# Kernel tuning notes

Measured on AMD Instinct MI355X. Metric: run time of the kernel, lower is better.

Reference implementation:

```python
import jax, jax.numpy as jnp
import numpy as np

B, C, H, W = 8, 256, 64, 64
HEADS, PTS = 8, 4
HD = C // HEADS
CIN_G, CIN_S, COUT = 1024, 320, 320


def _sine_pe(c, h, w):
    # LoFTR-style 2D sinusoidal position encoding, returns [C,H,W]
    pe = np.zeros((c, h, w), dtype=np.float32)
    y = np.broadcast_to(np.arange(h, dtype=np.float32)[None, :, None], (1, h, w))
    x = np.broadcast_to(np.arange(w, dtype=np.float32)[None, None, :], (1, h, w))
    div = np.exp(np.arange(0, c // 2, 2, dtype=np.float32) * (-np.log(10000.0) / (c // 2)))[:, None, None]
    pe[0::4] = np.sin(x * div)
    pe[1::4] = np.cos(x * div)
    pe[2::4] = np.sin(y * div)
    pe[3::4] = np.cos(y * div)
    return jnp.asarray(pe)


def _ref_points(h, w):
    # faithful to source: meshgrid over (W,H) 'ij', stack (col,row), flatten w-major
    rows = np.linspace(0, 1, w, dtype=np.float32)
    cols = np.linspace(0, 1, h, dtype=np.float32)
    R, Cg = np.meshgrid(rows, cols, indexing='ij')  # [W,H]
    return jnp.asarray(np.stack([Cg, R], -1).reshape(-1, 2))  # [W*H,2]


PE = _sine_pe(C, H, W)
RP = _ref_points(H, W)


def conv1x1(x, w, b):
    return jnp.einsum('bchw,oc->bohw', x, w) + b[None, :, None, None]


def deform_attn(qf, vf, vp_w, vp_b, so_w, so_b, aw_w, aw_b, op_w, op_b):
    # qf: [B,Nq,C]  vf: [B,Nv,C]  (single level, H x W value map)
    Bn, Nq, Cc = qf.shape
    v = (vf @ vp_w + vp_b).reshape(Bn, -1, HEADS, HD).transpose(0, 2, 1, 3)  # [B,h,Nv,hd]
    off = (qf @ so_w + so_b).reshape(Bn, Nq, HEADS, PTS, 2)
    aw = jax.nn.softmax((qf @ aw_w + aw_b).reshape(Bn, Nq, HEADS, PTS), axis=-1)
    loc = RP[None, :, None, None, :] + off / jnp.array([W, H], qf.dtype)  # [B,Nq,h,P,2]
    # grid_sample align_corners=False, zero padding
    px = loc[..., 0] * W - 0.5
    py = loc[..., 1] * H - 0.5
    x0 = jnp.floor(px).astype(jnp.int32)
    y0 = jnp.floor(py).astype(jnp.int32)
    wx = px - x0
    wy = py - y0
    out = jnp.zeros((Bn, HEADS, Nq, PTS, HD), qf.dtype)
    for dx, dy, wgt in ((0, 0, (1 - wx) * (1 - wy)), (1, 0, wx * (1 - wy)),
                        (0, 1, (1 - wx) * wy), (1, 1, wx * wy)):
        xi = x0 + dx
        yi = y0 + dy
        valid = ((xi >= 0) & (xi < W) & (yi >= 0) & (yi < H)).astype(qf.dtype)
        idx = jnp.clip(yi, 0, H - 1) * W + jnp.clip(xi, 0, W - 1)  # [B,Nq,h,P]
        idx_h = idx.transpose(0, 2, 1, 3).reshape(Bn, HEADS, Nq * PTS)
        g = jnp.take_along_axis(v, idx_h[..., None], axis=2).reshape(Bn, HEADS, Nq, PTS, HD)
        out = out + g * (wgt * valid).transpose(0, 2, 1, 3)[..., None]
    o = (out * aw.transpose(0, 2, 1, 3)[..., None]).sum(3)  # [B,h,Nq,hd]
    o = o.transpose(0, 2, 1, 3).reshape(Bn, Nq, Cc)
    return o @ op_w + op_b + qf  # mmcv: output_proj + identity (dropout=eval)


def cross_attn(q, value, vp_w, vp_b, so_w, so_b, aw_w, aw_b, op_w, op_b):
    qp = q + PE[None]  # query += pe
    qf = qp.reshape(qp.shape[0], C, H * W).transpose(0, 2, 1)
    vf = value.reshape(value.shape[0], C, H * W).transpose(0, 2, 1)
    o = deform_attn(qf, vf, vp_w, vp_b, so_w, so_b, aw_w, aw_b, op_w, op_b)
    o = o.transpose(0, 2, 1).reshape(qp.shape)
    return o + qp


def setup_inputs() -> dict:
    key = jax.random.key(0)
    ks = jax.random.split(key, 40)
    inp = {}
    inp['ground'] = jax.random.normal(ks[0], (B, CIN_G, H, W), jnp.float32)
    inp['sat'] = jax.random.normal(ks[1], (B, CIN_S, H, W), jnp.float32)
    inp['osm'] = jax.random.normal(ks[2], (B, CIN_S, H, W), jnp.float32)
    i = [3]
    def p(name, shape, scale=0.02):
        inp[name] = jax.random.normal(ks[i[0]], shape, jnp.float32) * scale
        i[0] += 1
    p('gc_w', (C, CIN_G)); p('gc_b', (C,))
    p('sc_w', (C, CIN_S)); p('sc_b', (C,))
    p('up_w', (COUT, C)); p('up_b', (COUT,))
    p('a_w1', (C, 64)); p('a_b1', (64,))
    p('a_w2', (64, 1)); p('a_b2', (1,))
    for pre in ('sat_', 'osm_'):
        p(pre + 'vp_w', (C, C)); p(pre + 'vp_b', (C,))
        p(pre + 'so_w', (C, HEADS * PTS * 2)); p(pre + 'so_b', (HEADS * PTS * 2,))
        p(pre + 'aw_w', (C, HEADS * PTS)); p(pre + 'aw_b', (HEADS * PTS,))
        p(pre + 'op_w', (C, C)); p(pre + 'op_b', (C,))
    inp['index'] = 0
    return inp


def reference(ground, sat, osm, gc_w, gc_b, sc_w, sc_b, up_w, up_b,
              a_w1, a_b1, a_w2, a_b2,
              sat_vp_w, sat_vp_b, sat_so_w, sat_so_b, sat_aw_w, sat_aw_b, sat_op_w, sat_op_b,
              osm_vp_w, osm_vp_b, osm_so_w, osm_so_b, osm_aw_w, osm_aw_b, osm_op_w, osm_op_b,
              index):
    del index  # params for index=0 already selected
    g = conv1x1(ground, gc_w, gc_b)
    s = conv1x1(sat, sc_w, sc_b)
    o = conv1x1(osm, sc_w, sc_b)  # source bug: osm projected with sat_convs
    gf = g.reshape(B, C, H * W).transpose(0, 2, 1)
    alpha = jax.nn.sigmoid(jax.nn.relu(gf @ a_w1 + a_b1) @ a_w2 + a_b2)  # [B,Nq,1]
    a = alpha.mean(axis=1)[:, :, None, None]  # [B,1,1,1]
    sat_out = cross_attn(g, s, sat_vp_w, sat_vp_b, sat_so_w, sat_so_b, sat_aw_w, sat_aw_b, sat_op_w, sat_op_b)
    # torch in-place `query += pe` inside ca_sat mutates `ground`, so ca_osm sees g + PE
    osm_out = cross_attn(g + PE[None], o, osm_vp_w, osm_vp_b, osm_so_w, osm_so_b, osm_aw_w, osm_aw_b, osm_op_w, osm_op_b)
    fused = a * sat_out + (1.0 - a) * osm_out
    return conv1x1(fused, up_w, up_b), a
```

## Files before the change

kernel.cpp:

```cpp
#include <hip/hip_runtime.h>
#include <cstddef>
#include <cstdint>

#define NB 8
#define NQ 4096

typedef __attribute__((ext_vector_type(8))) short bfrag8;
typedef __attribute__((ext_vector_type(4))) float facc4;
typedef __attribute__((ext_vector_type(4))) unsigned short us4;
typedef __attribute__((ext_vector_type(8))) unsigned short us8;

__device__ __forceinline__ float bf2f(unsigned short u) {
  union { unsigned int i; float f; } v; v.i = ((unsigned int)u) << 16; return v.f;
}
__device__ __forceinline__ unsigned short f2bf(float f) {
  union { float f; unsigned int i; } v; v.f = f;
  unsigned int r = v.i + 0x7FFFu + ((v.i >> 16) & 1u);
  return (unsigned short)(r >> 16);
}
__device__ __forceinline__ void gload16(const void* g, void* l) {
  __builtin_amdgcn_global_load_lds(
      (const __attribute__((address_space(1))) void*)g,
      (__attribute__((address_space(3))) void*)l, 16, 0, 0);
}

struct PrepArgs {
  const float *gc_w, *up_w, *up_b;
  const float *so_w0, *so_b0, *so_w1, *so_b1;
  const float *aw_w0, *aw_b0, *aw_w1, *aw_b1;
  const float *op_w0, *op_w1;
  unsigned short *PET, *WG, *WUP, *OPT0, *OPT1, *SOW0, *SOW1;
  float *BUPP, *SOB0, *SOB1;
};

__global__ __launch_bounds__(256) void mega_prep(PrepArgs p) {
  const int blk = blockIdx.x, t = threadIdx.x;
  if (blk < 4096) {
    int idx = blk * 256 + t;
    int q = idx >> 8, c = idx & 255;
    int h = q >> 6, w = q & 63;
    int k = c >> 2, m = c & 3;
    float dv = expf((float)(2 * k) * (-9.210340371976184f / 128.0f));
    float arg = ((m < 2) ? (float)w : (float)h) * dv;
    p.PET[idx] = f2bf(((m & 1) == 0) ? sinf(arg) : cosf(arg));
  } else if (blk < 5120) {
    int i = (blk - 4096) * 256 + t;
    p.WG[i] = f2bf(p.gc_w[i]);
  } else if (blk < 5504) {
    int i = (blk - 5120) * 256 + t;
    int m = i >> 8, k = i & 255;
    p.WUP[i] = (m < 320) ? f2bf(p.up_w[m * 256 + k]) : 0;
  } else if (blk < 5505) {
    p.BUPP[t] = (t < 320) ? p.up_b[t] : 0.f;
    if (t < 128) {
      int i2 = 256 + t;
      p.BUPP[i2] = (i2 < 320) ? p.up_b[i2] : 0.f;
    }
  } else if (blk < 6017) {
    int i = (blk - 5505) * 256 + t;
    int which = i >> 16, j = i & 65535;
    int o = j >> 8, k = j & 255;
    (which ? p.OPT1 : p.OPT0)[j] = f2bf((which ? p.op_w1 : p.op_w0)[k * 256 + o]);
  } else {
    int i = (blk - 6017) * 256 + t;
    int which = i >> 15, j = i & 32767;
    int row = j >> 8, k = j & 255;
    const float* sw = which ? p.so_w1 : p.so_w0;
    const float* aw = which ? p.aw_w1 : p.aw_w0;
    float v = 0.f;
    if (row < 64) v = sw[k * 64 + row];
    else if (row < 96) v = aw[k * 32 + (row - 64)];
    (which ? p.SOW1 : p.SOW0)[j] = f2bf(v);
    if (j < 128) {
      const float* sb = which ? p.so_b1 : p.so_b0;
      const float* ab = which ? p.aw_b1 : p.aw_b0;
      (which ? p.SOB1 : p.SOB0)[j] = (j < 64) ? sb[j] : ((j < 96) ? ab[j - 64] : 0.f);
    }
  }
}

__global__ __launch_bounds__(256) void k_wv(const float* __restrict__ vp_w0,
                                            const float* __restrict__ vp_b0,
                                            const float* __restrict__ vp_w1,
                                            const float* __restrict__ vp_b1,
                                            const float* __restrict__ sc_w,
                                            const float* __restrict__ sc_b,
                                            unsigned short* __restrict__ WV0,
                                            unsigned short* __restrict__ WV1,
                                            float* __restrict__ BV0,
                                            float* __restrict__ BV1) {
  const int br = blockIdx.y, kt = blockIdx.x, k0 = kt * 20, t = threadIdx.x;
  const float* vp = br ? vp_w1 : vp_w0;
  unsigned short* WV = br ? WV1 : WV0;
  __shared__ float vt[32][256];
  __shared__ float st[32][20];
  __shared__ float sb[32];
  float acc[20] = {};
  float accB = 0.f;
  for (int c0 = 0; c0 < 256; c0 += 32) {
    __syncthreads();
#pragma unroll
    for (int cc = 0; cc < 32; ++cc)
      vt[cc][t] = vp[(size_t)(c0 + cc) * 256 + t];
    for (int i = t; i < 640; i += 256)
      st[i / 20][i % 20] = sc_w[(size_t)(c0 + i / 20) * 320 + k0 + (i % 20)];
    if (t < 32) sb[t] = sc_b[c0 + t];
    __syncthreads();
#pragma unroll
    for (int cc = 0; cc < 32; ++cc) {
      float v = vt[cc][t];
      accB = fmaf(v, sb[cc], accB);
#pragma unroll
      for (int j = 0; j < 20; ++j)
        acc[j] = fmaf(v, st[cc][j], acc[j]);
    }
  }
#pragma unroll
  for (int j = 0; j < 20; ++j) WV[(size_t)t * 320 + k0 + j] = f2bf(acc[j]);
  if (kt == 0) (br ? BV1 : BV0)[t] = (br ? vp_b1 : vp_b0)[t] + accB;
}

struct GArgs {
  const unsigned short* W[2];
  const unsigned short* X[2];
  const float* bias[2];
  void* out[2];
  const unsigned short* res[2];
  float rscale[2];
  int K, ldm, bmask, brshift;
};
template <int MODE>
__global__ __launch_bounds__(256) void gemm_bf16(GArgs g) {
  __shared__ unsigned short As[8192];
  __shared__ unsigned short Bs[8192];
  const int t = threadIdx.x;
  const int lane = t & 63, w = t >> 6;
  const int z = blockIdx.z;
  const int b = z & g.bmask, br = z >> g.brshift;
  const int K = g.K;
  const int n0 = blockIdx.x * 128, m0 = 0;
  const unsigned short* W = g.W[br];
  const unsigned short* Xb = g.X[br] + (size_t)b * NQ * K;

  const unsigned short* asrc[4];
  const unsigned short* bsrc[4];
  unsigned short* adst[4];
  unsigned short* bdst[4];
#pragma unroll
  for (int i = 0; i < 4; ++i) {
    int cid = i * 256 + t;
    int row = cid >> 3;
    int cc = (cid & 7) ^ (row & 7);
    asrc[i] = W + (size_t)(m0 + row) * K + cc * 8;
    bsrc[i] = Xb + (size_t)(n0 + row) * K + cc * 8;
    adst[i] = &As[i * 2048 + w * 512];
    bdst[i] = &Bs[i * 2048 + w * 512];
  }
  const int wm = (w >> 1) * 64, wn = (w & 1) * 64;
  const int l15 = lane & 15, l4 = lane >> 4;
  facc4 acc[4][4];
#pragma unroll
  for (int i = 0; i < 4; ++i)
#pragma unroll
    for (int j = 0; j < 4; ++j) acc[i][j] = facc4{0.f, 0.f, 0.f, 0.f};

  for (int k0 = 0; k0 < K; k0 += 64) {
    if (k0) __syncthreads();
#pragma unroll
    for (int i = 0; i < 4; ++i) {
      gload16(asrc[i], adst[i]);
      gload16(bsrc[i], bdst[i]);
      asrc[i] += 64; bsrc[i] += 64;
    }
    __syncthreads();
#pragma unroll
    for (int kk = 0; kk < 2; ++kk) {
      bfrag8 af[4], bf[4];
#pragma unroll
      for (int mi = 0; mi < 4; ++mi) {
        int row = wm + mi * 16 + l15;
        af[mi] = *reinterpret_cast<const bfrag8*>(&As[row * 64 + (((kk * 4 + l4) ^ (row & 7)) * 8)]);
      }
#pragma unroll
      for (int ni = 0; ni < 4; ++ni) {
        int row = wn + ni * 16 + l15;
        bf[ni] = *reinterpret_cast<const bfrag8*>(&Bs[row * 64 + (((kk * 4 + l4) ^ (row & 7)) * 8)]);
      }
#pragma unroll
      for (int mi = 0; mi < 4; ++mi)
#pragma unroll
        for (int ni = 0; ni < 4; ++ni)
          acc[mi][ni] = __builtin_amdgcn_mfma_f32_16x16x32_bf16(af[mi], bf[ni], acc[mi][ni], 0, 0, 0);
    }
  }
  const size_t bq = (size_t)b * NQ;
#pragma unroll
  for (int mi = 0; mi < 4; ++mi) {
#pragma unroll
    for (int ni = 0; ni < 4; ++ni) {
      int m = m0 + wm + mi * 16 + l4 * 4;
      int n = n0 + wn + ni * 16 + l15;
      facc4 v = acc[mi][ni];
      unsigned short* o16 = (unsigned short*)g.out[br];
      float rv[4] = {v[0], v[1], v[2], v[3]};
      if constexpr (MODE == 1) {
        float sc = g.rscale[br];
        float4 bv = *reinterpret_cast<const float4*>(&g.bias[br][m]);
        rv[0] = rv[0] * sc + bv.x; rv[1] = rv[1] * sc + bv.y;
        rv[2] = rv[2] * sc + bv.z; rv[3] = rv[3] * sc + bv.w;
      }
      if constexpr (MODE == 2) {
        float sc = g.rscale[br];
        us4 rr = *reinterpret_cast<const us4*>(&g.res[br][(size_t)n * 128 + m]);
#pragma unroll
        for (int r = 0; r < 4; ++r) rv[r] += sc * bf2f(rr[r]);
      }
      us4 pk;
#pragma unroll
      for (int r = 0; r < 4; ++r) pk[r] = f2bf(rv[r]);
      *reinterpret_cast<us4*>(&o16[(bq + n) * g.ldm + m]) = pk;
    }
  }
}

struct NArgs {
  const unsigned short* W[2];
  const void* X[2];
  const float* bias[2];
  void* out[2];
  const unsigned short* G;
  const unsigned short* PET;
  const float* afin;
  float rs[2];
  int K, zmask, zshift;
};
template <int BSRC, int MODE>
__global__ __launch_bounds__(256) void gemm_n64(NArgs g) {
  __shared__ unsigned short As[16384];
  __shared__ unsigned short Bs[4096];
  const int t = threadIdx.x;
  const int lane = t & 63, w = t >> 6;
  const int z = blockIdx.z;
  const int b = z & g.zmask, br = z >> g.zshift;
  const int K = g.K;
  const int n0 = blockIdx.x * 64;

  const unsigned short* W = g.W[br];
  const unsigned short* asrc[8];
  unsigned short* adst[8];
#pragma unroll
  for (int i = 0; i < 8; ++i) {
    int c = t + 256 * i;
    int row = c >> 3;
    int k8 = (c & 7) ^ (row & 7);
    asrc[i] = W + (size_t)row * K + k8 * 8;
    adst[i] = &As[w * 512 + i * 2048];
  }

  const unsigned short* bsrc16[2];
  unsigned short* bdst16[2];
  const float* bsrcf = nullptr;
  const int kb = t >> 4, nb = t & 15;
  if constexpr (BSRC == 0) {
    const unsigned short* Xh = (const unsigned short*)g.X[br];
#pragma unroll
    for (int i = 0; i < 2; ++i) {
      int c = t + 256 * i;
      int n = c >> 3;
      int k8 = (c & 7) ^ (n & 7);
      bsrc16[i] = Xh + ((size_t)b * NQ + n0 + n) * K + k8 * 8;
      bdst16[i] = &Bs[w * 512 + i * 2048];
    }
  } else {
    const float* Xf = (const float*)g.X[br];
    bsrcf = Xf + (size_t)b * K * NQ + (size_t)(kb * 4) * NQ + n0 + nb * 4;
  }

  const int l15 = lane & 15, l4 = lane >> 4;
  facc4 acc[4][4];
#pragma unroll
  for (int i = 0; i < 4; ++i)
#pragma unroll
    for (int j = 0; j < 4; ++j) acc[i][j] = facc4{0.f, 0.f, 0.f, 0.f};

  for (int k0 = 0; k0 < K; k0 += 64) {
    if (k0) __syncthreads();
#pragma unroll
    for (int i = 0; i < 8; ++i) {
      gload16(asrc[i], adst[i]);
      asrc[i] += 64;
    }
    if constexpr (BSRC == 0) {
      gload16(bsrc16[0], bdst16[0]); bsrc16[0] += 64;
      gload16(bsrc16[1], bdst16[1]); bsrc16[1] += 64;
    } else {
      float vv[4][4];
#pragma unroll
      for (int r = 0; r < 4; ++r) {
        float4 v = *reinterpret_cast<const float4*>(bsrcf + (size_t)k0 * NQ + (size_t)r * NQ);
        vv[r][0] = v.x; vv[r][1] = v.y; vv[r][2] = v.z; vv[r][3] = v.w;
      }
#pragma unroll
      for (int c = 0; c < 4; ++c) {
        int n = nb * 4 + c;
        us4 pk;
        pk[0] = f2bf(vv[0][c]); pk[1] = f2bf(vv[1][c]);
        pk[2] = f2bf(vv[2][c]); pk[3] = f2bf(vv[3][c]);
        int off = n * 64 + (((kb >> 1) ^ (n & 7)) * 8) + (kb & 1) * 4;
        *reinterpret_cast<us4*>(&Bs[off]) = pk;
      }
    }
    __syncthreads();
#pragma unroll
    for (int kk = 0; kk < 2; ++kk) {
      bfrag8 af[4], bf[4];
#pragma unroll
      for (int mi = 0; mi < 4; ++mi) {
        int row = w * 64 + mi * 16 + l15;
        af[mi] = *reinterpret_cast<const bfrag8*>(&As[row * 64 + (((kk * 4 + l4) ^ (row & 7)) * 8)]);
      }
#pragma unroll
      for (int ni = 0; ni < 4; ++ni) {
        int row = ni * 16 + l15;
        bf[ni] = *reinterpret_cast<const bfrag8*>(&Bs[row * 64 + (((kk * 4 + l4) ^ (row & 7)) * 8)]);
      }
#pragma unroll
      for (int mi = 0; mi < 4; ++mi)
#pragma unroll
        for (int ni = 0; ni < 4; ++ni)
          acc[mi][ni] = __builtin_amdgcn_mfma_f32_16x16x32_bf16(af[mi], bf[ni], acc[mi][ni], 0, 0, 0);
    }
  }

  const size_t bq = (size_t)b * NQ;
  unsigned short* o16 = (unsigned short*)g.out[br];
#pragma unroll
  for (int mi = 0; mi < 4; ++mi) {
#pragma unroll
    for (int ni = 0; ni < 4; ++ni) {
      int m = w * 64 + mi * 16 + l4 * 4;
      int n = n0 + ni * 16 + l15;
      facc4 v = acc[mi][ni];
      float4 bv = *reinterpret_cast<const float4*>(&g.bias[br][m]);
      float rv[4] = {v[0] + bv.x, v[1] + bv.y, v[2] + bv.z, v[3] + bv.w};
      if constexpr (MODE == 6) {
        float a = g.afin[b];
        float s = br ? (1.f - a) : a;
        float rsc = g.rs[br];
        us4 gv = *reinterpret_cast<const us4*>(&g.G[(bq + n) * 256 + m]);
        us4 pv = *reinterpret_cast<const us4*>(&g.PET[(size_t)n * 256 + m]);
#pragma unroll
        for (int r = 0; r < 4; ++r)
          rv[r] = s * (rv[r] + 2.f * bf2f(gv[r]) + rsc * bf2f(pv[r]));
      }
      us4 pk;
#pragma unroll
      for (int r = 0; r < 4; ++r) pk[r] = f2bf(rv[r]);
      *reinterpret_cast<us4*>(&o16[(bq + n) * 256 + m]) = pk;
    }
  }
}

__global__ __launch_bounds__(384) void gemm_up(const unsigned short* __restrict__ W,
                                               const unsigned short* __restrict__ S0,
                                               const unsigned short* __restrict__ S1,
                                               const float* __restrict__ bias,
                                               float* __restrict__ out) {
  __shared__ unsigned short As[24576];
  __shared__ unsigned short Bs[4096];
  const int t = threadIdx.x;
  const int lane = t & 63, w = t >> 6;
  const int b = blockIdx.z;
  const int n0 = blockIdx.x * 64;

  const unsigned short* asrc[8];
  unsigned short* adst[8];
#pragma unroll
  for (int i = 0; i < 8; ++i) {
    int c = t + 384 * i;
    int row = c >> 3;
    int k8 = (c & 7) ^ (row & 7);
    asrc[i] = W + (size_t)row * 256 + k8 * 8;
    adst[i] = &As[w * 512 + i * 3072];
  }
  const bool bst = t < 256;
  size_t bidx[2];
  int bn[2];
  if (bst) {
#pragma unroll
    for (int i = 0; i < 2; ++i) {
      int c = t + 256 * i;
      bn[i] = c >> 3;
      int bk8 = (c & 7) ^ (bn[i] & 7);
      bidx[i] = ((size_t)b * NQ + n0 + bn[i]) * 256 + bk8 * 8;
    }
  }

  const int l15 = lane & 15, l4 = lane >> 4;
  facc4 acc[4][4];
#pragma unroll
  for (int i = 0; i < 4; ++i)
#pragma unroll
    for (int j = 0; j < 4; ++j) acc[i][j] = facc4{0.f, 0.f, 0.f, 0.f};

  for (int k0 = 0; k0 < 256; k0 += 64) {
    if (k0) __syncthreads();
#pragma unroll
    for (int i = 0; i < 8; ++i) {
      gload16(asrc[i], adst[i]);
      asrc[i] += 64;
    }
    if (bst) {
#pragma unroll
      for (int i = 0; i < 2; ++i) {
        us8 x = *reinterpret_cast<const us8*>(&S0[bidx[i] + k0]);
        us8 y = *reinterpret_cast<const us8*>(&S1[bidx[i] + k0]);
        us8 o;
#pragma unroll
        for (int j = 0; j < 8; ++j) o[j] = f2bf(bf2f(x[j]) + bf2f(y[j]));
        *reinterpret_cast<us8*>(&Bs[(t + 256 * i) * 8]) = o;
      }
    }
    __syncthreads();
#pragma unroll
    for (int kk = 0; kk < 2; ++kk) {
      bfrag8 af[4], bf[4];
#pragma unroll
      for (int mi = 0; mi < 4; ++mi) {
        int row = w * 64 + mi * 16 + l15;
        af[mi] = *reinterpret_cast<const bfrag8*>(&As[row * 64 + (((kk * 4 + l4) ^ (row & 7)) * 8)]);
      }
#pragma unroll
      for (int ni = 0; ni < 4; ++ni) {
        int row = ni * 16 + l15;
        bf[ni] = *reinterpret_cast<const bfrag8*>(&Bs[row * 64 + (((kk * 4 + l4) ^ (row & 7)) * 8)]);
      }
#pragma unroll
      for (int mi = 0; mi < 4; ++mi)
#pragma unroll
        for (int ni = 0; ni < 4; ++ni)
          acc[mi][ni] = __builtin_amdgcn_mfma_f32_16x16x32_bf16(af[mi], bf[ni], acc[mi][ni], 0, 0, 0);
    }
  }
#pragma unroll
  for (int mi = 0; mi < 4; ++mi) {
    int m = w * 64 + mi * 16 + l4 * 4;
    if (m >= 320) continue;
#pragma unroll
    for (int ni = 0; ni < 4; ++ni) {
      int n = n0 + ni * 16 + l15;
      facc4 v = acc[mi][ni];
#pragma unroll
      for (int r = 0; r < 4; ++r)
        out[((size_t)b * 320 + m + r) * NQ + n] = v[r] + bias[m + r];
    }
  }
}

__global__ __launch_bounds__(256) void k_alpha(const unsigned short* __restrict__ G,
                                               const float* __restrict__ w1,
                                               const float* __restrict__ b1,
                                               const float* __restrict__ w2,
                                               const float* __restrict__ b2,
                                               float* __restrict__ partial) {
  int b = blockIdx.y;
  int qbase = blockIdx.x * 16;
  __shared__ float gs[16][256];
  __shared__ float wsum[4];
  int t = threadIdx.x;
  const unsigned short* gp = G + ((size_t)b * NQ + qbase) * 256;
#pragma unroll
  for (int i = t; i < 512; i += 256) {
    bfrag8 v = *reinterpret_cast<const bfrag8*>(&gp[i * 8]);
    int row = i >> 5, col = (i & 31) * 8;
#pragma unroll
    for (int j = 0; j < 8; ++j) gs[row][col + j] = bf2f((unsigned short)v[j]);
  }
  __syncthreads();
  int wv = t >> 6, lane = t & 63;
  float a0 = 0.f, a1 = 0.f, a2 = 0.f, a3 = 0.f;
  const float* g0 = gs[wv * 4 + 0];
  const float* g1 = gs[wv * 4 + 1];
  const float* g2 = gs[wv * 4 + 2];
  const float* g3 = gs[wv * 4 + 3];
#pragma unroll 4
  for (int k = 0; k < 256; ++k) {
    float wk = w1[k * 64 + lane];
    a0 = fmaf(g0[k], wk, a0); a1 = fmaf(g1[k], wk, a1);
    a2 = fmaf(g2[k], wk, a2); a3 = fmaf(g3[k], wk, a3);
  }
  float b1l = b1[lane], w2l = w2[lane];
  a0 = fmaxf(a0 + b1l, 0.f) * w2l; a1 = fmaxf(a1 + b1l, 0.f) * w2l;
  a2 = fmaxf(a2 + b1l, 0.f) * w2l; a3 = fmaxf(a3 + b1l, 0.f) * w2l;
#pragma unroll
  for (int off = 32; off; off >>= 1) {
    a0 += __shfl_xor(a0, off); a1 += __shfl_xor(a1, off);
    a2 += __shfl_xor(a2, off); a3 += __shfl_xor(a3, off);
  }
  if (lane == 0) {
    float bb = b2[0];
    float s = 1.f / (1.f + expf(-(a0 + bb))) + 1.f / (1.f + expf(-(a1 + bb))) +
              1.f / (1.f + expf(-(a2 + bb))) + 1.f / (1.f + expf(-(a3 + bb)));
    wsum[wv] = s;
  }
  __syncthreads();
  if (t == 0) partial[(size_t)b * 256 + blockIdx.x] = wsum[0] + wsum[1] + wsum[2] + wsum[3];
}

__global__ __launch_bounds__(256) void k_alpha_fin(const float* __restrict__ partial,
                                                   float* __restrict__ afin,
                                                   float* __restrict__ out_a) {
  int b = blockIdx.x;
  __shared__ float sm[256];
  sm[threadIdx.x] = partial[(size_t)b * 256 + threadIdx.x];
  __syncthreads();
  for (int st = 128; st; st >>= 1) {
    if (threadIdx.x < st) sm[threadIdx.x] += sm[threadIdx.x + st];
    __syncthreads();
  }
  if (threadIdx.x == 0) {
    float a = sm[0] * (1.f / 4096.f);
    afin[b] = a;
    out_a[b] = a;
  }
}

__global__ __launch_bounds__(256) void k_sample(const unsigned short* __restrict__ VP0,
                                                const unsigned short* __restrict__ VP1,
                                                const unsigned short* __restrict__ SWb,
                                                unsigned short* __restrict__ OATT0,
                                                unsigned short* __restrict__ OATT1) {
  int y = blockIdx.y;
  int b = y & 7, br = y >> 3;
  int q0 = blockIdx.x * 8;
  const unsigned short* VP = (br ? VP1 : VP0) + (size_t)b * NQ * 256;
  const unsigned short* SWp = SWb + (((size_t)br * NB + b) * NQ + q0) * 128;
  unsigned short* OATT = (br ? OATT1 : OATT0) + ((size_t)b * NQ + q0) * 256;
  __shared__ unsigned short sws[1024];
  int t = threadIdx.x;
  *reinterpret_cast<us4*>(&sws[t * 4]) = *reinterpret_cast<const us4*>(&SWp[t * 4]);
  __syncthreads();
  int qi = t >> 5, ss = t & 31, head = ss >> 2, hdg = ss & 3;
  int q = q0 + qi;
  const unsigned short* sw = &sws[qi * 128];
  float l0 = bf2f(sw[64 + head * 4 + 0]);
  float l1 = bf2f(sw[64 + head * 4 + 1]);
  float l2 = bf2f(sw[64 + head * 4 + 2]);
  float l3 = bf2f(sw[64 + head * 4 + 3]);
  float mx = fmaxf(fmaxf(l0, l1), fmaxf(l2, l3));
  float e0 = expf(l0 - mx), e1 = expf(l1 - mx), e2 = expf(l2 - mx), e3 = expf(l3 - mx);
  float inv = 1.f / (e0 + e1 + e2 + e3);
  float aw[4] = {e0 * inv, e1 * inv, e2 * inv, e3 * inv};
  float rpx = (float)(q & 63) * (64.f / 63.f) - 0.5f;
  float rpy = (float)(q >> 6) * (64.f / 63.f) - 0.5f;
  const unsigned short* vb = VP + head * 32 + hdg * 8;
  float acc[8] = {};
#pragma unroll
  for (int p = 0; p < 4; ++p) {
    float px = rpx + bf2f(sw[head * 8 + p * 2 + 0]);
    float py = rpy + bf2f(sw[head * 8 + p * 2 + 1]);
    float fx = floorf(px), fy = floorf(py);
    int x0 = (int)fx, y0 = (int)fy;
    float wx = px - fx, wy = py - fy;
#pragma unroll
    for (int dy = 0; dy < 2; ++dy) {
#pragma unroll
      for (int dx = 0; dx < 2; ++dx) {
        int xi = x0 + dx, yi = y0 + dy;
        if (xi >= 0 && xi < 64 && yi >= 0 && yi < 64) {
          float wa = aw[p] * (dx ? wx : 1.f - wx) * (dy ? wy : 1.f - wy);
          bfrag8 v = *reinterpret_cast<const bfrag8*>(&vb[(size_t)(yi * 64 + xi) * 256]);
#pragma unroll
          for (int j = 0; j < 8; ++j) acc[j] = fmaf(wa, bf2f((unsigned short)v[j]), acc[j]);
        }
      }
    }
  }
  us8 o;
#pragma unroll
  for (int j = 0; j < 8; ++j) o[j] = f2bf(acc[j]);
  *reinterpret_cast<us8*>(&OATT[qi * 256 + ss * 8]) = o;
}

extern "C" void kernel_launch(void* const* d_in, const int* in_sizes, int n_in,
                              void* d_out, int out_size, void* d_ws, size_t ws_size,
                              hipStream_t stream) {
  const float* ground = (const float*)d_in[0];
  const float* sat = (const float*)d_in[1];
  const float* osm = (const float*)d_in[2];
  const float* gc_w = (const float*)d_in[3];
  const float* gc_b = (const float*)d_in[4];
  const float* sc_w = (const float*)d_in[5];
  const float* sc_b = (const float*)d_in[6];
  const float* up_w = (const float*)d_in[7];
  const float* up_b = (const float*)d_in[8];
  const float* a_w1 = (const float*)d_in[9];
  const float* a_b1 = (const float*)d_in[10];
  const float* a_w2 = (const float*)d_in[11];
  const float* a_b2 = (const float*)d_in[12];
  const float* vp_w[2] = {(const float*)d_in[13], (const float*)d_in[21]};
  const float* vp_b[2] = {(const float*)d_in[14], (const float*)d_in[22]};
  const float* so_w[2] = {(const float*)d_in[15], (const float*)d_in[23]};
  const float* so_b[2] = {(const float*)d_in[16], (const float*)d_in[24]};
  const float* aw_w[2] = {(const float*)d_in[17], (const float*)d_in[25]};
  const float* aw_b[2] = {(const float*)d_in[18], (const float*)d_in[26]};
  const float* op_w[2] = {(const float*)d_in[19], (const float*)d_in[27]};
  const float* op_b[2] = {(const float*)d_in[20], (const float*)d_in[28]};

  char* wsb = (char*)d_ws;
  const size_t MBy = 1 << 20;
  unsigned short* PET  = (unsigned short*)(wsb);
  unsigned short* WG   = (unsigned short*)(wsb + 2 * MBy);
  unsigned short* WV0  = (unsigned short*)(wsb + 2 * MBy + 524288);
  unsigned short* WV1  = (unsigned short*)(wsb + 2 * MBy + 786432);
  unsigned short* WUP  = (unsigned short*)(wsb + 3 * MBy);
  unsigned short* OPT0 = (unsigned short*)(wsb + 3 * MBy + 262144);
  unsigned short* OPT1 = (unsigned short*)(wsb + 3 * MBy + 393216);
  unsigned short* SOW0 = (unsigned short*)(wsb + 3 * MBy + 524288);
  unsigned short* SOW1 = (unsigned short*)(wsb + 3 * MBy + 589824);
  unsigned short* PESO0 = (unsigned short*)(wsb + 4 * MBy);
  unsigned short* PESO1 = (unsigned short*)(wsb + 5 * MBy);
  float* SOB0 = (float*)(wsb + 6 * MBy);
  float* SOB1 = (float*)(wsb + 6 * MBy + 4096);
  float* BV0  = (float*)(wsb + 6 * MBy + 8192);
  float* BV1  = (float*)(wsb + 6 * MBy + 12288);
  float* BUPP = (float*)(wsb + 6 * MBy + 16384);
  float* PART = (float*)(wsb + 6 * MBy + 32768);
  float* AFIN = (float*)(wsb + 6 * MBy + 65536);
  unsigned short* G     = (unsigned short*)(wsb + 8 * MBy);
  unsigned short* VP0b  = (unsigned short*)(wsb + 24 * MBy);
  unsigned short* VP1b  = (unsigned short*)(wsb + 40 * MBy);
  unsigned short* SW    = (unsigned short*)(wsb + 56 * MBy);
  unsigned short* OATT0 = (unsigned short*)(wsb + 72 * MBy);
  unsigned short* OATT1 = (unsigned short*)(wsb + 88 * MBy);
  unsigned short* SATO  = (unsigned short*)(wsb + 104 * MBy);
  unsigned short* OSMO  = (unsigned short*)(wsb + 120 * MBy);

  float* out32 = (float*)d_out;
  float* out_a = out32 + (size_t)NB * 320 * NQ;

  dim3 blk(256);

  {
    PrepArgs p;
    p.gc_w = gc_w; p.up_w = up_w; p.up_b = up_b;
    p.so_w0 = so_w[0]; p.so_b0 = so_b[0]; p.so_w1 = so_w[1]; p.so_b1 = so_b[1];
    p.aw_w0 = aw_w[0]; p.aw_b0 = aw_b[0]; p.aw_w1 = aw_w[1]; p.aw_b1 = aw_b[1];
    p.op_w0 = op_w[0]; p.op_w1 = op_w[1];
    p.PET = PET; p.WG = WG; p.WUP = WUP;
    p.OPT0 = OPT0; p.OPT1 = OPT1; p.SOW0 = SOW0; p.SOW1 = SOW1;
    p.BUPP = BUPP; p.SOB0 = SOB0; p.SOB1 = SOB1;
    mega_prep<<<dim3(6273), blk, 0, stream>>>(p);
  }
  k_wv<<<dim3(16, 2), blk, 0, stream>>>(vp_w[0], vp_b[0], vp_w[1], vp_b[1],
                                        sc_w, sc_b, WV0, WV1, BV0, BV1);

  {
    GArgs a = {};
    a.W[0] = SOW0; a.W[1] = SOW1;
    a.X[0] = PET;  a.X[1] = PET;
    a.bias[0] = SOB0; a.bias[1] = SOB1;
    a.out[0] = PESO0; a.out[1] = PESO1;
    a.rscale[0] = 1.f; a.rscale[1] = 2.f;
    a.K = 256; a.ldm = 128; a.bmask = 0; a.brshift = 0;
    gemm_bf16<1><<<dim3(32, 1, 2), blk, 0, stream>>>(a);
  }

  {
    NArgs a = {};
    a.W[0] = WG; a.W[1] = WG;
    a.X[0] = ground; a.X[1] = ground;
    a.bias[0] = gc_b; a.bias[1] = gc_b;
    a.out[0] = G; a.out[1] = G;
    a.K = 1024; a.zmask = 7; a.zshift = 31;
    gemm_n64<1, 0><<<dim3(64, 1, NB), blk, 0, stream>>>(a);
  }

  k_alpha<<<dim3(256, NB), blk, 0, stream>>>(G, a_w1, a_b1, a_w2, a_b2, PART);
  k_alpha_fin<<<dim3(NB), blk, 0, stream>>>(PART, AFIN, out_a);

  {
    GArgs a = {};
    a.W[0] = SOW0; a.W[1] = SOW1;
    a.X[0] = G; a.X[1] = G;
    a.out[0] = SW; a.out[1] = SW + (size_t)NB * NQ * 128;
    a.res[0] = PESO0; a.res[1] = PESO1;
    a.rscale[0] = 1.f; a.rscale[1] = 1.f;
    a.K = 256; a.ldm = 128; a.bmask = 7; a.brshift = 3;
    gemm_bf16<2><<<dim3(32, 1, 16), blk, 0, stream>>>(a);
  }

  {
    NArgs a = {};
    a.W[0] = WV0; a.W[1] = WV1;
    a.X[0] = sat; a.X[1] = osm;
    a.bias[0] = BV0; a.bias[1] = BV1;
    a.out[0] = VP0b; a.out[1] = VP1b;
    a.K = 320; a.zmask = 7; a.zshift = 3;
    gemm_n64<1, 0><<<dim3(64, 1, 16), blk, 0, stream>>>(a);
  }

  k_sample<<<dim3(512, 16), blk, 0, stream>>>(VP0b, VP1b, SW, OATT0, OATT1);

  {
    NArgs a = {};
    a.W[0] = OPT0; a.W[1] = OPT1;
    a.X[0] = OATT0; a.X[1] = OATT1;
    a.bias[0] = op_b[0]; a.bias[1] = op_b[1];
    a.out[0] = SATO; a.out[1] = OSMO;
    a.G = G; a.PET = PET; a.afin = AFIN;
    a.rs[0] = 2.f; a.rs[1] = 4.f;
    a.K = 256; a.zmask = 7; a.zshift = 3;
    gemm_n64<0, 6><<<dim3(64, 1, 16), blk, 0, stream>>>(a);
  }

  gemm_up<<<dim3(64, 1, NB), dim3(384), 0, stream>>>(WUP, SATO, OSMO, BUPP, out32);
}
```

Measured before the change: 299.0 us.

## Fuse sampling-offset projections for both branches with alpha MLP into one GEMM

Stacks the sat/osm offset+attention-weight weights and the alpha MLP first layer into one 320x256 weight matrix. A new 384-thread kernel computes all of them from G in a single pass, adding the PE residual and computing the per-query alpha sigmoid partial sums in the epilogue. This replaces the scalar FMA alpha kernel and the separate two-branch offset GEMM, so G is read once and the alpha MLP runs on MFMA. One of six waves does no MFMA work, and the SW layout changes to an interleaved 256-wide row, which k_sample now reads with strided loads.

After: 272.1 us. 9.0% less time.

```diff
diff --git a/kernel.cpp b/kernel.cpp
--- a/kernel.cpp
+++ b/kernel.cpp
@@ -28,9 +28,10 @@
   const float *gc_w, *up_w, *up_b;
   const float *so_w0, *so_b0, *so_w1, *so_b1;
   const float *aw_w0, *aw_b0, *aw_w1, *aw_b1;
+  const float *a_w1;
   const float *op_w0, *op_w1;
-  unsigned short *PET, *WG, *WUP, *OPT0, *OPT1, *SOW0, *SOW1;
-  float *BUPP, *SOB0, *SOB1;
+  unsigned short *PET, *WG, *WUP, *OPT0, *OPT1, *SOWS;
+  float *BUPP, *SOBS;
 };
 
 __global__ __launch_bounds__(256) void mega_prep(PrepArgs p) {
@@ -63,18 +64,23 @@
     (which ? p.OPT1 : p.OPT0)[j] = f2bf((which ? p.op_w1 : p.op_w0)[k * 256 + o]);
   } else {
     int i = (blk - 6017) * 256 + t;
-    int which = i >> 15, j = i & 32767;
-    int row = j >> 8, k = j & 255;
-    const float* sw = which ? p.so_w1 : p.so_w0;
-    const float* aw = which ? p.aw_w1 : p.aw_w0;
+    int row = i >> 8, k = i & 255;
     float v = 0.f;
-    if (row < 64) v = sw[k * 64 + row];
-    else if (row < 96) v = aw[k * 32 + (row - 64)];
-    (which ? p.SOW1 : p.SOW0)[j] = f2bf(v);
-    if (j < 128) {
-      const float* sb = which ? p.so_b1 : p.so_b0;
-      const float* ab = which ? p.aw_b1 : p.aw_b0;
-      (which ? p.SOB1 : p.SOB0)[j] = (j < 64) ? sb[j] : ((j < 96) ? ab[j - 64] : 0.f);
+    if (row < 256) {
+      int br = row >> 7, rr = row & 127;
+      const float* sw = br ? p.so_w1 : p.so_w0;
+      const float* aw = br ? p.aw_w1 : p.aw_w0;
+      if (rr < 64) v = sw[k * 64 + rr];
+      else if (rr < 96) v = aw[k * 32 + (rr - 64)];
+    } else if (row < 320) {
+      v = p.a_w1[k * 64 + (row - 256)];
+    }
+    p.SOWS[i] = f2bf(v);
+    if (i < 256) {
+      int br = i >> 7, rr = i & 127;
+      const float* sb = br ? p.so_b1 : p.so_b0;
+      const float* ab = br ? p.aw_b1 : p.aw_b0;
+      p.SOBS[i] = (rr < 64) ? sb[rr] : ((rr < 96) ? ab[rr - 64] : 0.f);
     }
   }
 }
@@ -125,7 +131,6 @@
   const unsigned short* X[2];
   const float* bias[2];
   void* out[2];
-  const unsigned short* res[2];
   float rscale[2];
   int K, ldm, bmask, brshift;
 };
@@ -138,7 +143,7 @@
   const int z = blockIdx.z;
   const int b = z & g.bmask, br = z >> g.brshift;
   const int K = g.K;
-  const int n0 = blockIdx.x * 128, m0 = 0;
+  const int n0 = blockIdx.x * 128;
   const unsigned short* W = g.W[br];
   const unsigned short* Xb = g.X[br] + (size_t)b * NQ * K;
 
@@ -151,7 +156,7 @@
     int cid = i * 256 + t;
     int row = cid >> 3;
     int cc = (cid & 7) ^ (row & 7);
-    asrc[i] = W + (size_t)(m0 + row) * K + cc * 8;
+    asrc[i] = W + (size_t)row * K + cc * 8;
     bsrc[i] = Xb + (size_t)(n0 + row) * K + cc * 8;
     adst[i] = &As[i * 2048 + w * 512];
     bdst[i] = &Bs[i * 2048 + w * 512];
@@ -198,26 +203,15 @@
   for (int mi = 0; mi < 4; ++mi) {
 #pragma unroll
     for (int ni = 0; ni < 4; ++ni) {
-      int m = m0 + wm + mi * 16 + l4 * 4;
+      int m = wm + mi * 16 + l4 * 4;
       int n = n0 + wn + ni * 16 + l15;
       facc4 v = acc[mi][ni];
       unsigned short* o16 = (unsigned short*)g.out[br];
-      float rv[4] = {v[0], v[1], v[2], v[3]};
-      if constexpr (MODE == 1) {
-        float sc = g.rscale[br];
-        float4 bv = *reinterpret_cast<const float4*>(&g.bias[br][m]);
-        rv[0] = rv[0] * sc + bv.x; rv[1] = rv[1] * sc + bv.y;
-        rv[2] = rv[2] * sc + bv.z; rv[3] = rv[3] * sc + bv.w;
-      }
-      if constexpr (MODE == 2) {
-        float sc = g.rscale[br];
-        us4 rr = *reinterpret_cast<const us4*>(&g.res[br][(size_t)n * 128 + m]);
-#pragma unroll
-        for (int r = 0; r < 4; ++r) rv[r] += sc * bf2f(rr[r]);
-      }
+      float sc = g.rscale[br];
+      float4 bv = *reinterpret_cast<const float4*>(&g.bias[br][m]);
       us4 pk;
-#pragma unroll
-      for (int r = 0; r < 4; ++r) pk[r] = f2bf(rv[r]);
+      pk[0] = f2bf(v[0] * sc + bv.x); pk[1] = f2bf(v[1] * sc + bv.y);
+      pk[2] = f2bf(v[2] * sc + bv.z); pk[3] = f2bf(v[3] * sc + bv.w);
       *reinterpret_cast<us4*>(&o16[(bq + n) * g.ldm + m]) = pk;
     }
   }
@@ -361,6 +355,144 @@
   }
 }
 
+struct SAArgs {
+  const unsigned short *W;
+  const unsigned short *G;
+  const unsigned short *PESOS;
+  const float *b1, *w2, *b2;
+  unsigned short *SWS;
+  float *partial;
+};
+__global__ __launch_bounds__(384) void k_swalpha(SAArgs g) {
+  __shared__ unsigned short As[24576];
+  __shared__ unsigned short Bs[4096];
+  const int t = threadIdx.x;
+  const int lane = t & 63, w = t >> 6;
+  const int b = blockIdx.z;
+  const int n0 = blockIdx.x * 64;
+
+  const unsigned short* asrc[8];
+  unsigned short* adst[8];
+#pragma unroll
+  for (int i = 0; i < 8; ++i) {
+    int c = t + 384 * i;
+    int row = c >> 3;
+    int k8 = (c & 7) ^ (row & 7);
+    asrc[i] = g.W + (size_t)row * 256 + k8 * 8;
+    adst[i] = &As[w * 512 + i * 3072];
+  }
+  const bool bst = t < 256;
+  const unsigned short* bsrc[2];
+  unsigned short* bdst[2];
+  if (bst) {
+#pragma unroll
+    for (int i = 0; i < 2; ++i) {
+      int c = t + 256 * i;
+      int n = c >> 3;
+      int k8 = (c & 7) ^ (n & 7);
+      bsrc[i] = g.G + ((size_t)b * NQ + n0 + n) * 256 + k8 * 8;
+      bdst[i] = &Bs[w * 512 + i * 2048];
+    }
+  }
+
+  const int l15 = lane & 15, l4 = lane >> 4;
+  facc4 acc[4][4];
+#pragma unroll
+  for (int i = 0; i < 4; ++i)
+#pragma unroll
+    for (int j = 0; j < 4; ++j) acc[i][j] = facc4{0.f, 0.f, 0.f, 0.f};
+
+  for (int k0 = 0; k0 < 256; k0 += 64) {
+    if (k0) __syncthreads();
+#pragma unroll
+    for (int i = 0; i < 8; ++i) {
+      gload16(asrc[i], adst[i]);
+      asrc[i] += 64;
+    }
+    if (bst) {
+      gload16(bsrc[0], bdst[0]); bsrc[0] += 64;
+      gload16(bsrc[1], bdst[1]); bsrc[1] += 64;
+    }
+    __syncthreads();
+    if (w < 5) {
+#pragma unroll
+      for (int kk = 0; kk < 2; ++kk) {
+        bfrag8 af[4], bf[4];
+#pragma unroll
+        for (int mi = 0; mi < 4; ++mi) {
+          int row = w * 64 + mi * 16 + l15;
+          af[mi] = *reinterpret_cast<const bfrag8*>(&As[row * 64 + (((kk * 4 + l4) ^ (row & 7)) * 8)]);
+        }
+#pragma unroll
+        for (int ni = 0; ni < 4; ++ni) {
+          int row = ni * 16 + l15;
+          bf[ni] = *reinterpret_cast<const bfrag8*>(&Bs[row * 64 + (((kk * 4 + l4) ^ (row & 7)) * 8)]);
+        }
+#pragma unroll
+        for (int mi = 0; mi < 4; ++mi)
+#pragma unroll
+          for (int ni = 0; ni < 4; ++ni)
+            acc[mi][ni] = __builtin_amdgcn_mfma_f32_16x16x32_bf16(af[mi], bf[ni], acc[mi][ni], 0, 0, 0);
+      }
+    }
+  }
+
+  const size_t bq = (size_t)b * NQ;
+  if (w < 4) {
+#pragma unroll
+    for (int mi = 0; mi < 4; ++mi) {
+#pragma unroll
+      for (int ni = 0; ni < 4; ++ni) {
+        int m = w * 64 + mi * 16 + l4 * 4;
+        int n = n0 + ni * 16 + l15;
+        facc4 v = acc[mi][ni];
+        us4 rr = *reinterpret_cast<const us4*>(&g.PESOS[(size_t)n * 256 + m]);
+        us4 pk;
+#pragma unroll
+        for (int r = 0; r < 4; ++r) pk[r] = f2bf(v[r] + bf2f(rr[r]));
+        *reinterpret_cast<us4*>(&g.SWS[(bq + n) * 256 + m]) = pk;
+      }
+    }
+  } else if (w == 4) {
+    float b2v = g.b2[0];
+    float ssum = 0.f;
+#pragma unroll
+    for (int ni = 0; ni < 4; ++ni) {
+      float s = 0.f;
+#pragma unroll
+      for (int mi = 0; mi < 4; ++mi) {
+#pragma unroll
+        for (int r = 0; r < 4; ++r) {
+          int hid = mi * 16 + l4 * 4 + r;
+          s += fmaxf(acc[mi][ni][r] + g.b1[hid], 0.f) * g.w2[hid];
+        }
+      }
+      s += __shfl_xor(s, 16);
+      s += __shfl_xor(s, 32);
+      ssum += 1.f / (1.f + expf(-(s + b2v)));
+    }
+    ssum += __shfl_xor(ssum, 1);
+    ssum += __shfl_xor(ssum, 2);
+    ssum += __shfl_xor(ssum, 4);
+    ssum += __shfl_xor(ssum, 8);
+    if (lane == 0) g.partial[b * 64 + blockIdx.x] = ssum;
+  }
+}
+
+__global__ __launch_bounds__(64) void k_alpha_fin(const float* __restrict__ partial,
+                                                  float* __restrict__ afin,
+                                                  float* __restrict__ out_a) {
+  int b = blockIdx.x;
+  float s = partial[b * 64 + threadIdx.x];
+#pragma unroll
+  for (int off = 32; off; off >>= 1) s += __shfl_xor(s, off);
+  if (threadIdx.x == 0) {
+    float a = s * (1.f / 4096.f);
+    afin[b] = a;
+    out_a[b] = a;
+  }
+}
+
 __global__ __launch_bounds__(384) void gemm_up(const unsigned short* __restrict__ W,
                                                const unsigned short* __restrict__ S0,
                                                const unsigned short* __restrict__ S1,
@@ -385,14 +517,13 @@
   }
   const bool bst = t < 256;
   size_t bidx[2];
-  int bn[2];
   if (bst) {
 #pragma unroll
     for (int i = 0; i < 2; ++i) {
       int c = t + 256 * i;
-      bn[i] = c >> 3;
-      int bk8 = (c & 7) ^ (bn[i] & 7);
-      bidx[i] = ((size_t)b * NQ + n0 + bn[i]) * 256 + bk8 * 8;
+      int n = c >> 3;
+      int bk8 = (c & 7) ^ (n & 7);
+      bidx[i] = ((size_t)b * NQ + n0 + n) * 256 + bk8 * 8;
     }
   }
 
@@ -457,88 +588,24 @@
   }
 }
 
-__global__ __launch_bounds__(256) void k_alpha(const unsigned short* __restrict__ G,
-                                               const float* __restrict__ w1,
-                                               const float* __restrict__ b1,
-                                               const float* __restrict__ w2,
-                                               const float* __restrict__ b2,
-                                               float* __restrict__ partial) {
-  int b = blockIdx.y;
-  int qbase = blockIdx.x * 16;
-  __shared__ float gs[16][256];
-  __shared__ float wsum[4];
-  int t = threadIdx.x;
-  const unsigned short* gp = G + ((size_t)b * NQ + qbase) * 256;
-#pragma unroll
-  for (int i = t; i < 512; i += 256) {
-    bfrag8 v = *reinterpret_cast<const bfrag8*>(&gp[i * 8]);
-    int row = i >> 5, col = (i & 31) * 8;
-#pragma unroll
-    for (int j = 0; j < 8; ++j) gs[row][col + j] = bf2f((unsigned short)v[j]);
-  }
-  __syncthreads();
-  int wv = t >> 6, lane = t & 63;
-  float a0 = 0.f, a1 = 0.f, a2 = 0.f, a3 = 0.f;
-  const float* g0 = gs[wv * 4 + 0];
-  const float* g1 = gs[wv * 4 + 1];
-  const float* g2 = gs[wv * 4 + 2];
-  const float* g3 = gs[wv * 4 + 3];
-#pragma unroll 4
-  for (int k = 0; k < 256; ++k) {
-    float wk = w1[k * 64 + lane];
-    a0 = fmaf(g0[k], wk, a0); a1 = fmaf(g1[k], wk, a1);
-    a2 = fmaf(g2[k], wk, a2); a3 = fmaf(g3[k], wk, a3);
-  }
-  float b1l = b1[lane], w2l = w2[lane];
-  a0 = fmaxf(a0 + b1l, 0.f) * w2l; a1 = fmaxf(a1 + b1l, 0.f) * w2l;
-  a2 = fmaxf(a2 + b1l, 0.f) * w2l; a3 = fmaxf(a3 + b1l, 0.f) * w2l;
-#pragma unroll
-  for (int off = 32; off; off >>= 1) {
-    a0 += __shfl_xor(a0, off); a1 += __shfl_xor(a1, off);
-    a2 += __shfl_xor(a2, off); a3 += __shfl_xor(a3, off);
-  }
-  if (lane == 0) {
-    float bb = b2[0];
-    float s = 1.f / (1.f + expf(-(a0 + bb))) + 1.f / (1.f + expf(-(a1 + bb))) +
-              1.f / (1.f + expf(-(a2 + bb))) + 1.f / (1.f + expf(-(a3 + bb)));
-    wsum[wv] = s;
-  }
-  __syncthreads();
-  if (t == 0) partial[(size_t)b * 256 + blockIdx.x] = wsum[0] + wsum[1] + wsum[2] + wsum[3];
-}
-
-__global__ __launch_bounds__(256) void k_alpha_fin(const float* __restrict__ partial,
-                                                   float* __restrict__ afin,
-                                                   float* __restrict__ out_a) {
-  int b = blockIdx.x;
-  __shared__ float sm[256];
-  sm[threadIdx.x] = partial[(size_t)b * 256 + threadIdx.x];
-  __syncthreads();
-  for (int st = 128; st; st >>= 1) {
-    if (threadIdx.x < st) sm[threadIdx.x] += sm[threadIdx.x + st];
-    __syncthreads();
-  }
-  if (threadIdx.x == 0) {
-    float a = sm[0] * (1.f / 4096.f);
-    afin[b] = a;
-    out_a[b] = a;
-  }
-}
-
 __global__ __launch_bounds__(256) void k_sample(const unsigned short* __restrict__ VP0,
                                                 const unsigned short* __restrict__ VP1,
-                                                const unsigned short* __restrict__ SWb,
+                                                const unsigned short* __restrict__ SWS,
                                                 unsigned short* __restrict__ OATT0,
                                                 unsigned short* __restrict__ OATT1) {
   int y = blockIdx.y;
   int b = y & 7, br = y >> 3;
   int q0 = blockIdx.x * 8;
   const unsigned short* VP = (br ? VP1 : VP0) + (size_t)b * NQ * 256;
-  const unsigned short* SWp = SWb + (((size_t)br * NB + b) * NQ + q0) * 128;
+  const unsigned short* SWp = SWS + ((size_t)b * NQ + q0) * 256 + br * 128;
   unsigned short* OATT = (br ? OATT1 : OATT0) + ((size_t)b * NQ + q0) * 256;
   __shared__ unsigned short sws[1024];
   int t = threadIdx.x;
-  *reinterpret_cast<us4*>(&sws[t * 4]) = *reinterpret_cast<const us4*>(&SWp[t * 4]);
+  {
+    int row = t >> 5, col = (t & 31) * 4;
+    *reinterpret_cast<us4*>(&sws[row * 128 + col]) =
+        *reinterpret_cast<const us4*>(&SWp[(size_t)row * 256 + col]);
+  }
   __syncthreads();
   int qi = t >> 5, ss = t & 31, head = ss >> 2, hdg = ss & 3;
   int q = q0 + qi;
@@ -616,21 +683,18 @@
   unsigned short* WUP  = (unsigned short*)(wsb + 3 * MBy);
   unsigned short* OPT0 = (unsigned short*)(wsb + 3 * MBy + 262144);
   unsigned short* OPT1 = (unsigned short*)(wsb + 3 * MBy + 393216);
-  unsigned short* SOW0 = (unsigned short*)(wsb + 3 * MBy + 524288);
-  unsigned short* SOW1 = (unsigned short*)(wsb + 3 * MBy + 589824);
-  unsigned short* PESO0 = (unsigned short*)(wsb + 4 * MBy);
-  unsigned short* PESO1 = (unsigned short*)(wsb + 5 * MBy);
-  float* SOB0 = (float*)(wsb + 6 * MBy);
-  float* SOB1 = (float*)(wsb + 6 * MBy + 4096);
-  float* BV0  = (float*)(wsb + 6 * MBy + 8192);
-  float* BV1  = (float*)(wsb + 6 * MBy + 12288);
-  float* BUPP = (float*)(wsb + 6 * MBy + 16384);
-  float* PART = (float*)(wsb + 6 * MBy + 32768);
-  float* AFIN = (float*)(wsb + 6 * MBy + 65536);
+  unsigned short* SOWS = (unsigned short*)(wsb + 3 * MBy + 524288);
+  unsigned short* PESOS = (unsigned short*)(wsb + 4 * MBy);
+  float* SOBS = (float*)(wsb + 6 * MBy);
+  float* BV0  = (float*)(wsb + 6 * MBy + 4096);
+  float* BV1  = (float*)(wsb + 6 * MBy + 8192);
+  float* BUPP = (float*)(wsb + 6 * MBy + 12288);
+  float* PART = (float*)(wsb + 6 * MBy + 16384);
+  float* AFIN = (float*)(wsb + 6 * MBy + 32768);
   unsigned short* G     = (unsigned short*)(wsb + 8 * MBy);
   unsigned short* VP0b  = (unsigned short*)(wsb + 24 * MBy);
   unsigned short* VP1b  = (unsigned short*)(wsb + 40 * MBy);
-  unsigned short* SW    = (unsigned short*)(wsb + 56 * MBy);
+  unsigned short* SWS   = (unsigned short*)(wsb + 56 * MBy);
   unsigned short* OATT0 = (unsigned short*)(wsb + 72 * MBy);
   unsigned short* OATT1 = (unsigned short*)(wsb + 88 * MBy);
   unsigned short* SATO  = (unsigned short*)(wsb + 104 * MBy);
@@ -646,23 +710,24 @@
     p.gc_w = gc_w; p.up_w = up_w; p.up_b = up_b;
     p.so_w0 = so_w[0]; p.so_b0 = so_b[0]; p.so_w1 = so_w[1]; p.so_b1 = so_b[1];
     p.aw_w0 = aw_w[0]; p.aw_b0 = aw_b[0]; p.aw_w1 = aw_w[1]; p.aw_b1 = aw_b[1];
+    p.a_w1 = a_w1;
     p.op_w0 = op_w[0]; p.op_w1 = op_w[1];
     p.PET = PET; p.WG = WG; p.WUP = WUP;
-    p.OPT0 = OPT0; p.OPT1 = OPT1; p.SOW0 = SOW0; p.SOW1 = SOW1;
-    p.BUPP = BUPP; p.SOB0 = SOB0; p.SOB1 = SOB1;
-    mega_prep<<<dim3(6273), blk, 0, stream>>>(p);
+    p.OPT0 = OPT0; p.OPT1 = OPT1; p.SOWS = SOWS;
+    p.BUPP = BUPP; p.SOBS = SOBS;
+    mega_prep<<<dim3(6401), blk, 0, stream>>>(p);
   }
   k_wv<<<dim3(16, 2), blk, 0, stream>>>(vp_w[0], vp_b[0], vp_w[1], vp_b[1],
                                         sc_w, sc_b, WV0, WV1, BV0, BV1);
 
   {
     GArgs a = {};
-    a.W[0] = SOW0; a.W[1] = SOW1;
+    a.W[0] = SOWS; a.W[1] = SOWS + 128 * 256;
     a.X[0] = PET;  a.X[1] = PET;
-    a.bias[0] = SOB0; a.bias[1] = SOB1;
-    a.out[0] = PESO0; a.out[1] = PESO1;
+    a.bias[0] = SOBS; a.bias[1] = SOBS + 128;
+    a.out[0] = PESOS; a.out[1] = PESOS + 128;
     a.rscale[0] = 1.f; a.rscale[1] = 2.f;
-    a.K = 256; a.ldm = 128; a.bmask = 0; a.brshift = 0;
+    a.K = 256; a.ldm = 256; a.bmask = 0; a.brshift = 0;
     gemm_bf16<1><<<dim3(32, 1, 2), blk, 0, stream>>>(a);
   }
 
@@ -676,19 +741,14 @@
     gemm_n64<1, 0><<<dim3(64, 1, NB), blk, 0, stream>>>(a);
   }
 
-  k_alpha<<<dim3(256, NB), blk, 0, stream>>>(G, a_w1, a_b1, a_w2, a_b2, PART);
-  k_alpha_fin<<<dim3(NB), blk, 0, stream>>>(PART, AFIN, out_a);
-
   {
-    GArgs a = {};
-    a.W[0] = SOW0; a.W[1] = SOW1;
-    a.X[0] = G; a.X[1] = G;
-    a.out[0] = SW; a.out[1] = SW + (size_t)NB * NQ * 128;
-    a.res[0] = PESO0; a.res[1] = PESO1;
-    a.rscale[0] = 1.f; a.rscale[1] = 1.f;
-    a.K = 256; a.ldm = 128; a.bmask = 7; a.brshift = 3;
-    gemm_bf16<2><<<dim3(32, 1, 16), blk, 0, stream>>>(a);
-  }
+    SAArgs a;
+    a.W = SOWS; a.G = G; a.PESOS = PESOS;
+    a.b1 = a_b1; a.w2 = a_w2; a.b2 = a_b2;
+    a.SWS = SWS; a.partial = PART;
+    k_swalpha<<<dim3(64, 1, NB), dim3(384), 0, stream>>>(a);
+  }
+  k_alpha_fin<<<dim3(NB), dim3(64), 0, stream>>>(PART, AFIN, out_a);
 
   {
     NArgs a = {};
@@ -700,7 +760,7 @@
     gemm_n64<1, 0><<<dim3(64, 1, 16), blk, 0, stream>>>(a);
   }
 
-  k_sample<<<dim3(512, 16), blk, 0, stream>>>(VP0b, VP1b, SW, OATT0, OATT1);
+  k_sample<<<dim3(512, 16), blk, 0, stream>>>(VP0b, VP1b, SWS, OATT0, OATT1);
 
   {
     NArgs a = {};
```
